# Performance work log

Measured on AMD Instinct MI355X. Metric: run time of the kernel, lower is better.

Reference implementation:

```python
import jax, jax.numpy as jnp
import numpy as np

B, P, H, W, D, C = 16, 4, 32, 32, 32, 8


def setup_inputs() -> dict:
    key = jax.random.key(0)
    k1, k2 = jax.random.split(key)
    input_fmap = jax.random.normal(k1, (B, P, H, W, D, C), dtype=jnp.float32)
    # identity affine + small noise so sampled coords mostly stay in-volume
    ident = jnp.concatenate([jnp.eye(3, dtype=jnp.float32), jnp.zeros((3, 1), jnp.float32)], axis=1)
    theta = ident[None, None] + 0.05 * jax.random.normal(k2, (B, P, 3, 4), dtype=jnp.float32)
    return {"input_fmap": input_fmap, "theta": theta}


def _affine_grid(theta, H, W, D):
    # matches tf.meshgrid default 'xy' indexing: shapes (H, W, D)
    x = jnp.arange(W, dtype=jnp.float32)
    y = jnp.arange(H, dtype=jnp.float32)
    z = jnp.arange(D, dtype=jnp.float32)
    xt, yt, zt = jnp.meshgrid(x, y, z, indexing='xy')  # each (H, W, D)
    grid = jnp.stack([xt.ravel(), yt.ravel(), zt.ravel(), jnp.ones(H * W * D, jnp.float32)], axis=0)  # (4, HWD)
    bg = jnp.einsum('bpij,jn->bpin', theta, grid)  # (B, P, 3, HWD)
    return bg.reshape(theta.shape[0], theta.shape[1], 3, H, W, D)


def reference(input_fmap, theta):
    Bb, Pp, Hh, Ww, Dd, Cc = input_fmap.shape
    bg = _affine_grid(theta, Hh, Ww, Dd)
    x = bg[:, :, 0] + 2.0  # (B, P, H, W, D)
    y = bg[:, :, 1] + 2.0
    z = bg[:, :, 2] + 2.0
    padded = jnp.pad(input_fmap, ((0, 0), (0, 0), (2, 2), (2, 2), (2, 2), (0, 0)))
    # faithful to original: all three axes clipped with H+2 (cubic volume assumed)
    x0 = jnp.clip(jnp.floor(x).astype(jnp.int32), 0, Hh + 2)
    y0 = jnp.clip(jnp.floor(y).astype(jnp.int32), 0, Hh + 2)
    z0 = jnp.clip(jnp.floor(z).astype(jnp.int32), 0, Hh + 2)
    x1, y1, z1 = x0 + 1, y0 + 1, z0 + 1

    bi = jnp.arange(Bb)[:, None, None, None, None]
    pi = jnp.arange(Pp)[None, :, None, None, None]

    def gather(xi, yi, zi):
        # (B, P, H, W, D, C), indices applied to spatial dims with batch_dims=2
        return padded[bi, pi, xi, yi, zi]

    c000 = gather(x0, y0, z0)
    c001 = gather(x0, y0, z1)
    c010 = gather(x0, y1, z0)
    c011 = gather(x0, y1, z1)
    c100 = gather(x1, y0, z0)
    c101 = gather(x1, y0, z1)
    c110 = gather(x1, y1, z0)
    c111 = gather(x1, y1, z1)

    xd = (x - x0.astype(jnp.float32))[..., None]  # (B, P, H, W, D, 1)
    yd = (y - y0.astype(jnp.float32))[..., None]
    zd = (z - z0.astype(jnp.float32))[..., None]

    out = (c000 * (1 - xd) * (1 - yd) * (1 - zd)
           + c100 * xd * (1 - yd) * (1 - zd)
           + c010 * (1 - xd) * yd * (1 - zd)
           + c001 * (1 - xd) * (1 - yd) * zd
           + c101 * xd * (1 - yd) * zd
           + c011 * (1 - xd) * yd * zd
           + c110 * xd * yd * (1 - zd)
           + c111 * xd * yd * zd)
    return out
```

## Files before the change

### kernel.cpp

```cpp
#include <hip/hip_runtime.h>
#include <cstddef>

#define BB 16
#define PP 4
#define HH 32
#define WW 32
#define DD 32
#define CC 8

__global__ __launch_bounds__(256) void resample_kernel(
    const float* __restrict__ fmap,
    const float* __restrict__ theta,
    float* __restrict__ out)
{
    const int bp  = blockIdx.x >> 7;
    const int vox = ((blockIdx.x & 127) << 8) | threadIdx.x;
    const int d = vox & 31;
    const int w = (vox >> 5) & 31;
    const int h = vox >> 10;

    const float* th = theta + bp * 12;
    const float fw = (float)w, fh = (float)h, fd = (float)d;
    const float x = fmaf(th[0], fw, fmaf(th[1], fh, fmaf(th[2],  fd, th[3] ))) + 2.0f;
    const float y = fmaf(th[4], fw, fmaf(th[5], fh, fmaf(th[6],  fd, th[7] ))) + 2.0f;
    const float z = fmaf(th[8], fw, fmaf(th[9], fh, fmaf(th[10], fd, th[11]))) + 2.0f;

    int x0 = min(max((int)floorf(x), 0), HH + 2);
    int y0 = min(max((int)floorf(y), 0), HH + 2);
    int z0 = min(max((int)floorf(z), 0), HH + 2);
    const float xd = x - (float)x0, yd = y - (float)y0, zd = z - (float)z0;
    const float xm = 1.0f - xd,     ym = 1.0f - yd,     zm = 1.0f - zd;

    const int ix0 = x0 - 2, iy0 = y0 - 2, iz0 = z0 - 2;
    const float* __restrict__ base = fmap + (size_t)bp * (HH * WW * DD * CC);

    float4 aA = make_float4(0.f, 0.f, 0.f, 0.f);
    float4 aB = make_float4(0.f, 0.f, 0.f, 0.f);

    #pragma unroll
    for (int cx = 0; cx < 2; ++cx) {
        const int ix = ix0 + cx;
        const bool vx = (unsigned)ix < (unsigned)HH;
        const float wx = cx ? xd : xm;
        #pragma unroll
        for (int cy = 0; cy < 2; ++cy) {
            const int iy = iy0 + cy;
            const bool vxy = vx && ((unsigned)iy < (unsigned)WW);
            const float wxy = wx * (cy ? yd : ym);
            #pragma unroll
            for (int cz = 0; cz < 2; ++cz) {
                const int iz = iz0 + cz;
                const float wgt = wxy * (cz ? zd : zm);
                if (vxy && ((unsigned)iz < (unsigned)DD)) {
                    const float4* p = (const float4*)(base + (size_t)(((ix * WW + iy) * DD + iz) * CC));
                    const float4 a = p[0];
                    const float4 b = p[1];
                    aA.x = fmaf(wgt, a.x, aA.x);
                    aA.y = fmaf(wgt, a.y, aA.y);
                    aA.z = fmaf(wgt, a.z, aA.z);
                    aA.w = fmaf(wgt, a.w, aA.w);
                    aB.x = fmaf(wgt, b.x, aB.x);
                    aB.y = fmaf(wgt, b.y, aB.y);
                    aB.z = fmaf(wgt, b.z, aB.z);
                    aB.w = fmaf(wgt, b.w, aB.w);
                }
            }
        }
    }

    float4* o = (float4*)(out + (size_t)(bp * (HH * WW * DD) + vox) * CC);
    o[0] = aA;
    o[1] = aB;
}

extern "C" void kernel_launch(void* const* d_in, const int* in_sizes, int n_in,
                              void* d_out, int out_size, void* d_ws, size_t ws_size,
                              hipStream_t stream) {
    const float* fmap  = (const float*)d_in[0];
    const float* theta = (const float*)d_in[1];
    float* out = (float*)d_out;

    const int total_blocks = BB * PP * ((HH * WW * DD) / 256);
    resample_kernel<<<dim3(total_blocks), dim3(256), 0, stream>>>(fmap, theta, out);
}
```

Measured before the change: 137.6 us.

## Split channels across thread pairs and make gathers branchless with clamped indices

Each voxel is now handled by two threads, each loading and blending one float4 half of the 8 channels, which doubles the thread count and halves per-thread work. Out-of-range corners are handled by clamping indices and zeroing weights instead of branching, so all eight loads can be issued up front without divergence. Output uses nontemporal stores. This adds duplicate coordinate math per thread pair and always issues eight loads, even for corners outside the volume.

```diff
diff --git a/kernel.cpp b/kernel.cpp
--- a/kernel.cpp
+++ b/kernel.cpp
@@ -8,13 +8,17 @@
 #define DD 32
 #define CC 8
 
+typedef float fx4 __attribute__((ext_vector_type(4)));
+
 __global__ __launch_bounds__(256) void resample_kernel(
     const float* __restrict__ fmap,
     const float* __restrict__ theta,
     float* __restrict__ out)
 {
-    const int bp  = blockIdx.x >> 7;
-    const int vox = ((blockIdx.x & 127) << 8) | threadIdx.x;
+    const int bp   = blockIdx.x >> 8;
+    const int tid  = threadIdx.x;
+    const int vox  = ((blockIdx.x & 255) << 7) | (tid >> 1);
+    const int half = tid & 1;
     const int d = vox & 31;
     const int w = (vox >> 5) & 31;
     const int h = vox >> 10;
@@ -25,52 +29,47 @@
     const float y = fmaf(th[4], fw, fmaf(th[5], fh, fmaf(th[6],  fd, th[7] ))) + 2.0f;
     const float z = fmaf(th[8], fw, fmaf(th[9], fh, fmaf(th[10], fd, th[11]))) + 2.0f;
 
-    int x0 = min(max((int)floorf(x), 0), HH + 2);
-    int y0 = min(max((int)floorf(y), 0), HH + 2);
-    int z0 = min(max((int)floorf(z), 0), HH + 2);
+    const int x0 = min(max((int)floorf(x), 0), HH + 2);
+    const int y0 = min(max((int)floorf(y), 0), HH + 2);
+    const int z0 = min(max((int)floorf(z), 0), HH + 2);
     const float xd = x - (float)x0, yd = y - (float)y0, zd = z - (float)z0;
-    const float xm = 1.0f - xd,     ym = 1.0f - yd,     zm = 1.0f - zd;
 
-    const int ix0 = x0 - 2, iy0 = y0 - 2, iz0 = z0 - 2;
-    const float* __restrict__ base = fmap + (size_t)bp * (HH * WW * DD * CC);
+    const int ix[2] = { x0 - 2, x0 - 1 };
+    const int iy[2] = { y0 - 2, y0 - 1 };
+    const int iz[2] = { z0 - 2, z0 - 1 };
+    const float wxv[2] = { (1.0f - xd) * (((unsigned)ix[0] < (unsigned)HH) ? 1.0f : 0.0f),
+                           xd          * (((unsigned)ix[1] < (unsigned)HH) ? 1.0f : 0.0f) };
+    const float wyv[2] = { (1.0f - yd) * (((unsigned)iy[0] < (unsigned)WW) ? 1.0f : 0.0f),
+                           yd          * (((unsigned)iy[1] < (unsigned)WW) ? 1.0f : 0.0f) };
+    const float wzv[2] = { (1.0f - zd) * (((unsigned)iz[0] < (unsigned)DD) ? 1.0f : 0.0f),
+                           zd          * (((unsigned)iz[1] < (unsigned)DD) ? 1.0f : 0.0f) };
+    const int cx[2] = { min(max(ix[0], 0), HH - 1), min(max(ix[1], 0), HH - 1) };
+    const int cy[2] = { min(max(iy[0], 0), WW - 1), min(max(iy[1], 0), WW - 1) };
+    const int cz[2] = { min(max(iz[0], 0), DD - 1), min(max(iz[1], 0), DD - 1) };
 
-    float4 aA = make_float4(0.f, 0.f, 0.f, 0.f);
-    float4 aB = make_float4(0.f, 0.f, 0.f, 0.f);
+    const float* __restrict__ base = fmap + (size_t)bp * (HH * WW * DD * CC) + half * 4;
 
+    fx4   c[8];
+    float wgt[8];
     #pragma unroll
-    for (int cx = 0; cx < 2; ++cx) {
-        const int ix = ix0 + cx;
-        const bool vx = (unsigned)ix < (unsigned)HH;
-        const float wx = cx ? xd : xm;
-        #pragma unroll
-        for (int cy = 0; cy < 2; ++cy) {
-            const int iy = iy0 + cy;
-            const bool vxy = vx && ((unsigned)iy < (unsigned)WW);
-            const float wxy = wx * (cy ? yd : ym);
-            #pragma unroll
-            for (int cz = 0; cz < 2; ++cz) {
-                const int iz = iz0 + cz;
-                const float wgt = wxy * (cz ? zd : zm);
-                if (vxy && ((unsigned)iz < (unsigned)DD)) {
-                    const float4* p = (const float4*)(base + (size_t)(((ix * WW + iy) * DD + iz) * CC));
-                    const float4 a = p[0];
-                    const float4 b = p[1];
-                    aA.x = fmaf(wgt, a.x, aA.x);
-                    aA.y = fmaf(wgt, a.y, aA.y);
-                    aA.z = fmaf(wgt, a.z, aA.z);
-                    aA.w = fmaf(wgt, a.w, aA.w);
-                    aB.x = fmaf(wgt, b.x, aB.x);
-                    aB.y = fmaf(wgt, b.y, aB.y);
-                    aB.z = fmaf(wgt, b.z, aB.z);
-                    aB.w = fmaf(wgt, b.w, aB.w);
-                }
-            }
-        }
+    for (int i = 0; i < 8; ++i) {
+        const int bx = (i >> 2) & 1, by = (i >> 1) & 1, bz = i & 1;
+        const size_t off = (size_t)(((cx[bx] * WW + cy[by]) * DD + cz[bz]) * CC);
+        c[i]   = *(const fx4*)(base + off);
+        wgt[i] = wxv[bx] * wyv[by] * wzv[bz];
     }
 
-    float4* o = (float4*)(out + (size_t)(bp * (HH * WW * DD) + vox) * CC);
-    o[0] = aA;
-    o[1] = aB;
+    fx4 acc = (fx4){0.f, 0.f, 0.f, 0.f};
+    #pragma unroll
+    for (int i = 0; i < 8; ++i) {
+        acc.x = fmaf(wgt[i], c[i].x, acc.x);
+        acc.y = fmaf(wgt[i], c[i].y, acc.y);
+        acc.z = fmaf(wgt[i], c[i].z, acc.z);
+        acc.w = fmaf(wgt[i], c[i].w, acc.w);
+    }
+
+    fx4* o = (fx4*)(out + (size_t)(bp * (HH * WW * DD) + vox) * CC + half * 4);
+    __builtin_nontemporal_store(acc, o);
 }
 
 extern "C" void kernel_launch(void* const* d_in, const int* in_sizes, int n_in,
@@ -80,6 +79,6 @@
     const float* theta = (const float*)d_in[1];
     float* out = (float*)d_out;
 
-    const int total_blocks = BB * PP * ((HH * WW * DD) / 256);
+    const int total_blocks = BB * PP * 256;
     resample_kernel<<<dim3(total_blocks), dim3(256), 0, stream>>>(fmap, theta, out);
 }
```

Result: faster. 122.4 us (-11.0%).
